# Optimization experiments

Measured on AMD Instinct MI355X. Metric: run time of the kernel, lower is better.

The kernel has to match this reference:

```python
import jax, jax.numpy as jnp
import numpy as np

N_DST = 25000
E = 400000
DN = 128   # dim_node
DE = 128   # dim_edge
DT = 128   # dim_time
DO = 128   # dim_out
H = 2      # num_head


def setup_inputs() -> dict:
    key = jax.random.key(0)
    ks = jax.random.split(key, 10)
    sc = 0.05
    node_h = jax.random.normal(ks[0], (N_DST + E, DN), jnp.float32)
    edge_f = jax.random.normal(ks[1], (E, DE), jnp.float32)
    dt = jax.random.uniform(ks[2], (E,), jnp.float32) * 100.0
    dst_idx = jax.random.randint(ks[3], (E,), 0, N_DST)
    # TimeEncode: Linear(1, dim_time) with w initialized to 1/10**linspace(0,9)
    time_w = jnp.asarray(1.0 / 10 ** np.linspace(0, 9, DT, dtype=np.float32))
    time_b = jnp.zeros((DT,), jnp.float32)
    Wq = jax.random.normal(ks[4], (DO, DN + DT), jnp.float32) * sc
    bq = jnp.zeros((DO,), jnp.float32)
    Wk = jax.random.normal(ks[5], (DO, DN + DE + DT), jnp.float32) * sc
    bk = jnp.zeros((DO,), jnp.float32)
    Wv = jax.random.normal(ks[6], (DO, DN + DE + DT), jnp.float32) * sc
    bv = jnp.zeros((DO,), jnp.float32)
    Wout = jax.random.normal(ks[7], (DO, DN + DO), jnp.float32) * sc
    bout = jnp.zeros((DO,), jnp.float32)
    gamma = jnp.ones((DO,), jnp.float32)
    beta = jnp.zeros((DO,), jnp.float32)
    return dict(node_h=node_h, edge_f=edge_f, dt=dt, dst_idx=dst_idx,
                time_w=time_w, time_b=time_b, Wq=Wq, bq=bq, Wk=Wk, bk=bk,
                Wv=Wv, bv=bv, Wout=Wout, bout=bout, gamma=gamma, beta=beta)


def reference(node_h, edge_f, dt, dst_idx, time_w, time_b,
              Wq, bq, Wk, bk, Wv, bv, Wout, bout, gamma, beta):
    num_dst = node_h.shape[0] - edge_f.shape[0]
    num_edges = edge_f.shape[0]
    tgt = node_h[:num_dst]            # [N, DN] target node embeddings
    src = node_h[num_dst:]            # [E, DN] per-edge source embeddings

    # TimeEncode: cos(w * dt + b)
    time_feats = jnp.cos(dt[:, None] * time_w[None, :] + time_b)          # [E, DT]
    zero_time = jnp.broadcast_to(jnp.cos(time_b), (num_dst, time_b.shape[0]))

    Qn = jnp.concatenate([tgt, zero_time], axis=1) @ Wq.T + bq            # [N, DO]
    kv_in = jnp.concatenate([src, edge_f, time_feats], axis=1)            # [E, DN+DE+DT]
    K = kv_in @ Wk.T + bk                                                 # [E, DO]
    V = kv_in @ Wv.T + bv                                                 # [E, DO]
    Q = Qn[dst_idx]                                                       # gather per edge

    d_head = Q.shape[1] // H
    Qh = Q.reshape(num_edges, H, d_head)
    Kh = K.reshape(num_edges, H, d_head)
    Vh = V.reshape(num_edges, H, d_head)

    score = jnp.sum(Qh * Kh, axis=2)                                      # [E, H]
    score = jnp.where(score >= 0, score, 0.2 * score)                     # LeakyReLU(0.2)

    # edge_softmax: segmented softmax over incoming edges of each dst node
    m = jax.ops.segment_max(score, dst_idx, num_segments=num_dst)
    m = jnp.where(jnp.isfinite(m), m, 0.0)                                # empty segments
    e = jnp.exp(score - m[dst_idx])
    s = jax.ops.segment_sum(e, dst_idx, num_segments=num_dst)
    att = e / s[dst_idx]                                                  # [E, H]

    Vw = (Vh * att[:, :, None]).reshape(num_edges, -1)                    # [E, DO]
    h = jax.ops.segment_sum(Vw, dst_idx, num_segments=num_dst)            # scatter-sum

    rst = jnp.concatenate([h, tgt], axis=1) @ Wout.T + bout               # [N, DO]
    rst = jax.nn.relu(rst)
    mu = jnp.mean(rst, axis=-1, keepdims=True)
    var = jnp.var(rst, axis=-1, keepdims=True)
    return (rst - mu) / jnp.sqrt(var + 1e-5) * gamma + beta
```

## Files before the change

kernel.cpp:

```cpp
#include <hip/hip_runtime.h>

#define N_DST 25000
#define E_NUM 400000

typedef __bf16 bf16x8 __attribute__((ext_vector_type(8)));
typedef __bf16 bf16x4 __attribute__((ext_vector_type(4)));
typedef float  f32x4  __attribute__((ext_vector_type(4)));

__device__ __forceinline__ float fast_cos(float x) {
  float r = x * 0.15915494309189535f;
  r = r - floorf(r);
  return __builtin_amdgcn_cosf(r);
}

__device__ __forceinline__ void pack_frag(const float* __restrict__ W0,
    const float* __restrict__ W1, int stride, int NC, int idx, __bf16* __restrict__ out) {
  int lane = idx & 63, fid = idx >> 6;
  int nfw = NC >> 6;
  int perks = nfw << 2;
  int ks = fid / perks, rem = fid - ks * perks;
  int w = rem / nfw, nf = rem - w * nfw;
  int n = w * (NC >> 2) + nf * 16 + (lane & 15);
  int g = (ks << 2) + (lane >> 4);
  const float* src = (W1 && n >= 128) ? (W1 + (size_t)(n - 128) * stride)
                                      : (W0 + (size_t)n * stride);
  const float4* s4 = reinterpret_cast<const float4*>(src + g * 8);
  float4 lo = s4[0], hi = s4[1];
  bf16x8 b;
  b[0]=(__bf16)lo.x; b[1]=(__bf16)lo.y; b[2]=(__bf16)lo.z; b[3]=(__bf16)lo.w;
  b[4]=(__bf16)hi.x; b[5]=(__bf16)hi.y; b[6]=(__bf16)hi.z; b[7]=(__bf16)hi.w;
  reinterpret_cast<bf16x8*>(out)[idx] = b;
}

__global__ __launch_bounds__(256) void prep_kernel(
    const float* __restrict__ Wq, const float* __restrict__ bq, const float* __restrict__ tb,
    const float* __restrict__ Wk, const float* __restrict__ Wv, const float* __restrict__ Wout,
    const int* __restrict__ dsti,
    float* __restrict__ cq, __bf16* __restrict__ Bq_kv, __bf16* __restrict__ Bq_q,
    __bf16* __restrict__ Bq_out, int* __restrict__ counts) {
  int b = blockIdx.x, tid = threadIdx.x;
  if (b == 0) {
    if (tid < 128) {
      float s = bq[tid];
      for (int j = 0; j < 128; ++j) s += cosf(tb[j]) * Wq[tid * 256 + 128 + j];
      cq[tid] = s;
    }
    return;
  }
  b -= 1;
  if (b < 48) { pack_frag(Wk, Wv, 384, 256, b * 256 + tid, Bq_kv); return; }
  b -= 48;
  if (b < 8)  { pack_frag(Wq, nullptr, 256, 128, b * 256 + tid, Bq_q); return; }
  b -= 8;
  if (b < 16) { pack_frag(Wout, nullptr, 256, 128, b * 256 + tid, Bq_out); return; }
  b -= 16;
  int e = b * 256 + tid;
  if (e < E_NUM) atomicAdd(&counts[dsti[e]], 1);
}

__global__ __launch_bounds__(1024) void scanA_kernel(const int* __restrict__ counts,
    int* __restrict__ bsum) {
  __shared__ int wsum[16];
  int tid = threadIdx.x;
  int idx = blockIdx.x * 1024 + tid;
  int s = (idx < N_DST) ? counts[idx] : 0;
#pragma unroll
  for (int o = 32; o; o >>= 1) s += __shfl_xor(s, o);
  if ((tid & 63) == 0) wsum[tid >> 6] = s;
  __syncthreads();
  if (tid == 0) {
    int t = 0;
#pragma unroll
    for (int i = 0; i < 16; ++i) t += wsum[i];
    bsum[blockIdx.x] = t;
  }
}

__global__ void scanB_kernel(const int* __restrict__ bsum, int* __restrict__ boff) {
  if (threadIdx.x == 0) {
    int c = 0;
    for (int i = 0; i < 25; ++i) { boff[i] = c; c += bsum[i]; }
    boff[25] = c;
  }
}

__global__ __launch_bounds__(1024) void scanC_kernel(const int* __restrict__ counts,
    const int* __restrict__ boff, int* __restrict__ offs, int* __restrict__ cursor) {
  __shared__ int wpart[16];
  int tid = threadIdx.x, lane = tid & 63, wid = tid >> 6;
  int idx = blockIdx.x * 1024 + tid;
  int x = (idx < N_DST) ? counts[idx] : 0;
  int incl = x;
#pragma unroll
  for (int o = 1; o < 64; o <<= 1) {
    int y = __shfl_up(incl, o);
    if (lane >= o) incl += y;
  }
  if (lane == 63) wpart[wid] = incl;
  __syncthreads();
  if (wid == 0) {
    int v = (lane < 16) ? wpart[lane] : 0;
    int s = v;
#pragma unroll
    for (int o = 1; o < 16; o <<= 1) {
      int y = __shfl_up(s, o);
      if (lane >= o) s += y;
    }
    if (lane < 16) wpart[lane] = s;
  }
  __syncthreads();
  int woff = (wid > 0) ? wpart[wid - 1] : 0;
  int v = boff[blockIdx.x] + woff + incl - x;
  if (idx < N_DST) {
    offs[idx] = v;
    cursor[idx] = v;
  }
  if (idx == N_DST - 1) offs[N_DST] = v + x;
}

__global__ __launch_bounds__(256) void fill_kernel(const int* __restrict__ dsti,
    int* __restrict__ cursor, int* __restrict__ elist, int* __restrict__ dsts) {
  int e = blockIdx.x * 256 + threadIdx.x;
  if (e < E_NUM) {
    int d = dsti[e];
    int p = atomicAdd(&cursor[d], 1);
    elist[p] = e;
    dsts[p] = d;
  }
}

#define WAITV(N) do { \
    asm volatile("s_waitcnt vmcnt(" #N ")" ::: "memory"); \
    __builtin_amdgcn_sched_barrier(0); } while (0)
#define PIPE_BAR() do { \
    asm volatile("s_waitcnt lgkmcnt(0)" ::: "memory"); \
    __builtin_amdgcn_sched_barrier(0); \
    __builtin_amdgcn_s_barrier(); \
    __builtin_amdgcn_sched_barrier(0); } while (0)

__global__ __launch_bounds__(256, 3) void kv_kernel(
    const float* __restrict__ node_h, const float* __restrict__ edge_f,
    const float* __restrict__ dtp, const float* __restrict__ tw, const float* __restrict__ tb,
    const __bf16* __restrict__ Bq,
    const float* __restrict__ bk, const float* __restrict__ bv,
    const int* __restrict__ elist, const int* __restrict__ dsts,
    const float* __restrict__ Qn,
    __bf16* __restrict__ Vout, float* __restrict__ score)
{
  __shared__ __align__(16) char SMEM[16384];
  __shared__ int Elds[64];
  __shared__ int Dlds[64];
  __shared__ float dts[64];
  __shared__ float twl[128];
  __shared__ float tbl[128];

  char* const Ab0 = SMEM;
  char* const Ab1 = SMEM + 8192;
  char* const Vlds = SMEM;

  const int tid = threadIdx.x;
  const int e0 = blockIdx.x * 64;
  const int lane = tid & 63;
  const int w = tid >> 6;
  const int lrow = lane & 15;
  const int lk = lane >> 4;
  const int aswz = (lrow & 7) << 4;

  if (tid < 64) {
    int e = elist[e0 + tid];
    Elds[tid] = e;
    Dlds[tid] = dsts[e0 + tid];
    dts[tid] = dtp[e];
  } else if (tid < 192) {
    int j = tid - 64;
    twl[j] = tw[j];
    tbl[j] = tb[j];
  }
  __syncthreads();

  const int srow = tid >> 2;
  const int sq = tid & 3;
  const int eidx = Elds[srow];
  const char* sR = (const char*)(node_h + (size_t)(N_DST + eidx) * 128) + sq * 64;
  const char* eR = (const char*)(edge_f + (size_t)eidx * 128) + sq * 64;

  float4 sA0, sA1, sA2, sA3, sB0, sB1, sB2, sB3;
#define ISSUE_STAGE(S0, S1, S2, S3, T) do { \
    const char* _p = ((T) < 2) ? (sR + (T) * 256) : (eR + ((T) - 2) * 256); \
    asm volatile("global_load_dwordx4 %0, %4, off\n\t" \
                 "global_load_dwordx4 %1, %4, off offset:16\n\t" \
                 "global_load_dwordx4 %2, %4, off offset:32\n\t" \
                 "global_load_dwordx4 %3, %4, off offset:48" \
                 : "=&v"(S0), "=&v"(S1), "=&v"(S2), "=&v"(S3) : "v"(_p)); } while (0)

  auto writeAt = [&](char* buf, float4 v0, float4 v1, float4 v2, float4 v3) {
    char* rb = buf + srow * 128;
    int sw = (srow & 7) << 4;
    float4 vv[4] = {v0, v1, v2, v3};
#pragma unroll
    for (int i = 0; i < 4; ++i) {
      bf16x4 b;
      b[0]=(__bf16)vv[i].x; b[1]=(__bf16)vv[i].y; b[2]=(__bf16)vv[i].z; b[3]=(__bf16)vv[i].w;
      *reinterpret_cast<bf16x4*>(rb + ((sq * 32 + i * 8) ^ sw)) = b;
    }
  };

  const bf16x8* __restrict__ Bw = reinterpret_cast<const bf16x8*>(Bq) + (size_t)(w * 4) * 64 + lane;
  float4 bq0, bq1, bq2, bq3, bq4, bq5, bq6, bq7;
#define ISSUE_B4(B0, B1, B2, B3, K32) do { \
    const void* _p = (const void*)(Bw + (size_t)(K32) * 16 * 64); \
    asm volatile("global_load_dwordx4 %0, %4, off\n\t" \
                 "global_load_dwordx4 %1, %4, off offset:1024\n\t" \
                 "global_load_dwordx4 %2, %4, off offset:2048\n\t" \
                 "global_load_dwordx4 %3, %4, off offset:3072" \
                 : "=&v"(B0), "=&v"(B1), "=&v"(B2), "=&v"(B3) : "v"(_p)); } while (0)
#define ISSUE_B8(T) do { ISSUE_B4(bq0, bq1, bq2, bq3, (T) * 2); \
                         ISSUE_B4(bq4, bq5, bq6, bq7, (T) * 2 + 1); } while (0)

  f32x4 acc[4][4];
#pragma unroll
  for (int mf = 0; mf < 4; ++mf)
#pragma unroll
    for (int nf = 0; nf < 4; ++nf)
      acc[mf][nf] = (f32x4){0.f, 0.f, 0.f, 0.f};

  float dv[4];
#pragma unroll
  for (int mf = 0; mf < 4; ++mf) dv[mf] = dts[mf * 16 + lrow];

  auto mfmaTile = [&](const char* buf) {
#pragma unroll
    for (int ks = 0; ks < 2; ++ks) {
#pragma unroll
      for (int mf = 0; mf < 4; ++mf) {
        bf16x8 a = *reinterpret_cast<const bf16x8*>(
            buf + (mf * 16 + lrow) * 128 + ((ks * 64 + lk * 16) ^ aswz));
        acc[mf][0] = __builtin_amdgcn_mfma_f32_16x16x32_bf16(a, __builtin_bit_cast(bf16x8, ks ? bq4 : bq0), acc[mf][0], 0, 0, 0);
        acc[mf][1] = __builtin_amdgcn_mfma_f32_16x16x32_bf16(a, __builtin_bit_cast(bf16x8, ks ? bq5 : bq1), acc[mf][1], 0, 0, 0);
        acc[mf][2] = __builtin_amdgcn_mfma_f32_16x16x32_bf16(a, __builtin_bit_cast(bf16x8, ks ? bq6 : bq2), acc[mf][2], 0, 0, 0);
        acc[mf][3] = __builtin_amdgcn_mfma_f32_16x16x32_bf16(a, __builtin_bit_cast(bf16x8, ks ? bq7 : bq3), acc[mf][3], 0, 0, 0);
      }
    }
  };

  ISSUE_STAGE(sA0, sA1, sA2, sA3, 0);
  ISSUE_STAGE(sB0, sB1, sB2, sB3, 1);
  WAITV(4);
  writeAt(Ab0, sA0, sA1, sA2, sA3);
  PIPE_BAR();
  ISSUE_B8(0);
  ISSUE_STAGE(sA0, sA1, sA2, sA3, 2);
  WAITV(4);
  mfmaTile(Ab0);
  writeAt(Ab1, sB0, sB1, sB2, sB3);
  PIPE_BAR();
  ISSUE_B8(1);
  ISSUE_STAGE(sB0, sB1, sB2, sB3, 3);
  WAITV(4);
  mfmaTile(Ab1);
  writeAt(Ab0, sA0, sA1, sA2, sA3);
  PIPE_BAR();
  ISSUE_B8(2);
  WAITV(0);
  mfmaTile(Ab0);
  writeAt(Ab1, sB0, sB1, sB2, sB3);
  PIPE_BAR();
  ISSUE_B8(3);
  WAITV(0);
  mfmaTile(Ab1);

  ISSUE_B4(bq0, bq1, bq2, bq3, 8);
#pragma unroll
  for (int cs = 0; cs < 4; ++cs) {
    if (cs == 0) ISSUE_B4(bq4, bq5, bq6, bq7, 9);
    else if (cs == 1) ISSUE_B4(bq0, bq1, bq2, bq3, 10);
    else if (cs == 2) ISSUE_B4(bq4, bq5, bq6, bq7, 11);
    int J = cs * 32 + lk * 8;
    f32x4 w0 = *reinterpret_cast<const f32x4*>(twl + J);
    f32x4 w1 = *reinterpret_cast<const f32x4*>(twl + J + 4);
    f32x4 c0 = *reinterpret_cast<const f32x4*>(tbl + J);
    f32x4 c1 = *reinterpret_cast<const f32x4*>(tbl + J + 4);
    bf16x8 a[4];
#pragma unroll
    for (int mf = 0; mf < 4; ++mf) {
      float d = dv[mf];
#pragma unroll
      for (int j = 0; j < 4; ++j) {
        a[mf][j] = (__bf16)fast_cos(d * w0[j] + c0[j]);
        a[mf][4 + j] = (__bf16)fast_cos(d * w1[j] + c1[j]);
      }
    }
    if (cs < 3) { WAITV(4); } else { WAITV(0); }
    bool lo = !(cs & 1);
    bf16x8 b0 = __builtin_bit_cast(bf16x8, lo ? bq0 : bq4);
    bf16x8 b1 = __builtin_bit_cast(bf16x8, lo ? bq1 : bq5);
    bf16x8 b2 = __builtin_bit_cast(bf16x8, lo ? bq2 : bq6);
    bf16x8 b3 = __builtin_bit_cast(bf16x8, lo ? bq3 : bq7);
#pragma unroll
    for (int mf = 0; mf < 4; ++mf) {
      acc[mf][0] = __builtin_amdgcn_mfma_f32_16x16x32_bf16(a[mf], b0, acc[mf][0], 0, 0, 0);
      acc[mf][1] = __builtin_amdgcn_mfma_f32_16x16x32_bf16(a[mf], b1, acc[mf][1], 0, 0, 0);
      acc[mf][2] = __builtin_amdgcn_mfma_f32_16x16x32_bf16(a[mf], b2, acc[mf][2], 0, 0, 0);
      acc[mf][3] = __builtin_amdgcn_mfma_f32_16x16x32_bf16(a[mf], b3, acc[mf][3], 0, 0, 0);
    }
  }

  PIPE_BAR();

  if (w >= 2) {
#pragma unroll
    for (int nf = 0; nf < 4; ++nf) {
      int vcol = (w - 2) * 64 + nf * 16 + lrow;
      float bb = bv[vcol];
#pragma unroll
      for (int mf = 0; mf < 4; ++mf) {
#pragma unroll
        for (int r = 0; r < 4; ++r) {
          int row = mf * 16 + lk * 4 + r;
          *reinterpret_cast<__bf16*>(Vlds + row * 256 + ((vcol * 2) ^ ((row & 7) << 4))) =
              (__bf16)(acc[mf][nf][r] + bb);
        }
      }
    }
  } else {
    float bkv[4];
#pragma unroll
    for (int nf = 0; nf < 4; ++nf) bkv[nf] = bk[w * 64 + nf * 16 + lrow];
#pragma unroll
    for (int mf = 0; mf < 4; ++mf) {
      float qv[4][4];
#pragma unroll
      for (int r = 0; r < 4; ++r) {
        const float* qrow = Qn + ((size_t)Dlds[mf * 16 + lk * 4 + r] << 7) + w * 64 + lrow;
#pragma unroll
        for (int nf = 0; nf < 4; ++nf)
          qv[r][nf] = qrow[nf * 16];
      }
#pragma unroll
      for (int r = 0; r < 4; ++r) {
        int row = mf * 16 + lk * 4 + r;
        float s = 0.f;
#pragma unroll
        for (int nf = 0; nf < 4; ++nf)
          s += (acc[mf][nf][r] + bkv[nf]) * qv[r][nf];
        s += __shfl_xor(s, 1);
        s += __shfl_xor(s, 2);
        s += __shfl_xor(s, 4);
        s += __shfl_xor(s, 8);
        if (lrow == 0) {
          s = (s >= 0.f) ? s : 0.2f * s;
          score[((size_t)(e0 + row) << 1) + w] = s;
        }
      }
    }
  }
  __syncthreads();
#pragma unroll
  for (int i = 0; i < 4; ++i) {
    int c = tid + i * 256;
    int r = c >> 4, cb = (c & 15) << 4;
    bf16x8 vv = *reinterpret_cast<const bf16x8*>(Vlds + r * 256 + (cb ^ ((r & 7) << 4)));
    *reinterpret_cast<bf16x8*>(Vout + (((size_t)(e0 + r)) << 7) + (c & 15) * 8) = vv;
  }
}

template<int MODE>
__global__ __launch_bounds__(256, 4) void gemm_kernel(
    const float* __restrict__ A0, const float* __restrict__ A1,
    const float* __restrict__ dtp, const float* __restrict__ tw,
    const __bf16* __restrict__ Bq, const float* __restrict__ bias0,
    float* __restrict__ outF)
{
  constexpr int NC = 128;
  constexpr int NFRAGW = 2;
  __shared__ __align__(16) char Abuf[2][64 * 256];

  const int tid = threadIdx.x;
  const int e0 = blockIdx.x * 64;
  const int nv = min(64, N_DST - e0);
  const int srow = tid >> 5;
  const int sc4 = (tid & 31) << 2;

  const int lane = tid & 63;
  const int w = tid >> 6;
  const int nbase = w * (NC / 4);
  const int lrow = lane & 15;
  const int lk = lane >> 4;
  const int aswz = (lrow & 7) << 4;
  const bf16x8* __restrict__ Bw =
      reinterpret_cast<const bf16x8*>(Bq) + (size_t)(w * NFRAGW) * 64 + lane;

  f32x4 acc[4][NFRAGW];
#pragma unroll
  for (int mf = 0; mf < 4; ++mf)
#pragma unroll
    for (int nf = 0; nf < NFRAGW; ++nf)
      acc[mf][nf] = (f32x4){0.f, 0.f, 0.f, 0.f};

  auto issueA = [&](int t, float4 (&v)[8]) {
    const float* base = (t == 0) ? A0 : A1;
#pragma unroll
    for (int i = 0; i < 8; ++i) {
      int r = srow + i * 8;
      v[i] = (r < nv) ? *reinterpret_cast<const float4*>(base + (size_t)(e0 + r) * 128 + sc4)
                      : make_float4(0.f, 0.f, 0.f, 0.f);
    }
  };
  auto writeA = [&](char* buf, float4 (&v)[8]) {
#pragma unroll
    for (int i = 0; i < 8; ++i) {
      int r = srow + i * 8;
      bf16x4 b;
      b[0]=(__bf16)v[i].x; b[1]=(__bf16)v[i].y; b[2]=(__bf16)v[i].z; b[3]=(__bf16)v[i].w;
      *reinterpret_cast<bf16x4*>(buf + r * 256 + ((sc4 * 2) ^ ((r & 7) << 4))) = b;
    }
  };
  auto ktile = [&](const char* buf, int t) {
#pragma unroll
    for (int ks = 0; ks < 4; ++ks) {
      bf16x8 b[NFRAGW];
#pragma unroll
      for (int nf = 0; nf < NFRAGW; ++nf)
        b[nf] = Bw[((size_t)(t * 4 + ks) * 4 * NFRAGW + nf) * 64];
      bf16x8 a[4];
#pragma unroll
      for (int mf = 0; mf < 4; ++mf)
        a[mf] = *reinterpret_cast<const bf16x8*>(
            buf + (mf * 16 + lrow) * 256 + (((ks * 32 + lk * 8) * 2) ^ aswz));
#pragma unroll
      for (int nf = 0; nf < NFRAGW; ++nf)
#pragma unroll
        for (int mf = 0; mf < 4; ++mf)
          acc[mf][nf] = __builtin_amdgcn_mfma_f32_16x16x32_bf16(a[mf], b[nf], acc[mf][nf], 0, 0, 0);
    }
  };

  float4 v[8];
  issueA(0, v);
  writeA(Abuf[0], v);
  __syncthreads();
  if constexpr (MODE == 2) {
    issueA(1, v);
    ktile(Abuf[0], 0);
    writeA(Abuf[1], v);
    __syncthreads();
    ktile(Abuf[1], 1);
  } else {
    ktile(Abuf[0], 0);
  }

  if constexpr (MODE == 0) {
#pragma unroll
    for (int nf = 0; nf < NFRAGW; ++nf) {
      int col = nbase + nf * 16 + lrow;
      float bb = bias0[col];
#pragma unroll
      for (int mf = 0; mf < 4; ++mf) {
#pragma unroll
        for (int r = 0; r < 4; ++r) {
          int row = mf * 16 + lk * 4 + r;
          if (row < nv)
            outF[(size_t)(e0 + row) * 128 + col] = acc[mf][nf][r] + bb;
        }
      }
    }
  } else {
    const float* gammaP = dtp;
    const float* betaP = tw;
    float vals[NFRAGW][4][4];
#pragma unroll
    for (int nf = 0; nf < NFRAGW; ++nf) {
      float bb = bias0[nbase + nf * 16 + lrow];
#pragma unroll
      for (int mf = 0; mf < 4; ++mf)
#pragma unroll
        for (int r = 0; r < 4; ++r)
          vals[nf][mf][r] = fmaxf(acc[mf][nf][r] + bb, 0.f);
    }
    __syncthreads();
    float* sums = reinterpret_cast<float*>(Abuf[0]);
    float* sqs  = reinterpret_cast<float*>(Abuf[0]) + 256;
    float* stats = reinterpret_cast<float*>(Abuf[0]) + 512;
#pragma unroll
    for (int mf = 0; mf < 4; ++mf) {
#pragma unroll
      for (int r = 0; r < 4; ++r) {
        float s1 = vals[0][mf][r] + vals[1][mf][r];
        float s2 = vals[0][mf][r] * vals[0][mf][r] + vals[1][mf][r] * vals[1][mf][r];
#pragma unroll
        for (int o = 1; o < 16; o <<= 1) {
          s1 += __shfl_xor(s1, o);
          s2 += __shfl_xor(s2, o);
        }
        if (lrow == 0) {
          int row = mf * 16 + lk * 4 + r;
          sums[w * 64 + row] = s1;
          sqs[w * 64 + row] = s2;
        }
      }
    }
    __syncthreads();
    if (tid < 64) {
      float s = sums[tid] + sums[64 + tid] + sums[128 + tid] + sums[192 + tid];
      float q = sqs[tid] + sqs[64 + tid] + sqs[128 + tid] + sqs[192 + tid];
      float mean = s * (1.f / 128.f);
      float var = q * (1.f / 128.f) - mean * mean;
      stats[tid * 2] = mean;
      stats[tid * 2 + 1] = rsqrtf(var + 1e-5f);
    }
    __syncthreads();
#pragma unroll
    for (int nf = 0; nf < NFRAGW; ++nf) {
      int col = nbase + nf * 16 + lrow;
      float g = gammaP[col], bC = betaP[col];
#pragma unroll
      for (int mf = 0; mf < 4; ++mf) {
#pragma unroll
        for (int r = 0; r < 4; ++r) {
          int row = mf * 16 + lk * 4 + r;
          if (row < nv) {
            float mean = stats[row * 2], rs = stats[row * 2 + 1];
            outF[(size_t)(e0 + row) * 128 + col] = (vals[nf][mf][r] - mean) * rs * g + bC;
          }
        }
      }
    }
  }
}

__global__ __launch_bounds__(256) void agg_kernel(const int* __restrict__ offs,
    const float* __restrict__ score, const __bf16* __restrict__ V, float* __restrict__ h) {
  int d = blockIdx.x * 4 + (threadIdx.x >> 6);
  if (d >= N_DST) return;
  int lane = threadIdx.x & 63;
  int beg = offs[d], end = offs[d + 1];
  int n = end - beg;
  float m0 = -3.0e38f, m1 = -3.0e38f;
  for (int i = lane; i < n; i += 64) {
    float2 sc = *reinterpret_cast<const float2*>(score + 2 * (size_t)(beg + i));
    m0 = fmaxf(m0, sc.x); m1 = fmaxf(m1, sc.y);
  }
#pragma unroll
  for (int o = 32; o; o >>= 1) {
    m0 = fmaxf(m0, __shfl_xor(m0, o));
    m1 = fmaxf(m1, __shfl_xor(m1, o));
  }
  float s0 = 0.f, s1 = 0.f;
  for (int i = lane; i < n; i += 64) {
    float2 sc = *reinterpret_cast<const float2*>(score + 2 * (size_t)(beg + i));
    s0 += __expf(sc.x - m0); s1 += __expf(sc.y - m1);
  }
#pragma unroll
  for (int o = 32; o; o >>= 1) {
    s0 += __shfl_xor(s0, o);
    s1 += __shfl_xor(s1, o);
  }
  float inv0 = (n > 0) ? 1.f / s0 : 0.f;
  float inv1 = (n > 0) ? 1.f / s1 : 0.f;
  int q = lane >> 4, j = lane & 15;
  int hsel = j >> 3;
  float acc[8];
#pragma unroll
  for (int k2 = 0; k2 < 8; ++k2) acc[k2] = 0.f;
  for (int i0 = 0; i0 < n; i0 += 4) {
    int i = i0 + q;
    if (i < n) {
      size_t p = beg + i;
      float2 sc = *reinterpret_cast<const float2*>(score + 2 * p);
      float wgt = hsel ? __expf(sc.y - m1) * inv1 : __expf(sc.x - m0) * inv0;
      bf16x8 v = *reinterpret_cast<const bf16x8*>(V + (p << 7) + j * 8);
#pragma unroll
      for (int k2 = 0; k2 < 8; ++k2) acc[k2] += wgt * (float)v[k2];
    }
  }
#pragma unroll
  for (int k2 = 0; k2 < 8; ++k2) {
    acc[k2] += __shfl_xor(acc[k2], 16);
    acc[k2] += __shfl_xor(acc[k2], 32);
  }
  if (q == 0) {
    float4 lo = make_float4(acc[0], acc[1], acc[2], acc[3]);
    float4 hi = make_float4(acc[4], acc[5], acc[6], acc[7]);
    float* dst = h + ((size_t)d << 7) + j * 8;
    *reinterpret_cast<float4*>(dst) = lo;
    *reinterpret_cast<float4*>(dst + 4) = hi;
  }
}

extern "C" void kernel_launch(void* const* d_in, const int* in_sizes, int n_in,
                              void* d_out, int out_size, void* d_ws, size_t ws_size,
                              hipStream_t stream) {
  (void)in_sizes; (void)n_in; (void)out_size; (void)ws_size;
  const float* node_h = (const float*)d_in[0];
  const float* edge_f = (const float*)d_in[1];
  const float* dtp    = (const float*)d_in[2];
  const int*   dsti   = (const int*)d_in[3];
  const float* tw     = (const float*)d_in[4];
  const float* tb     = (const float*)d_in[5];
  const float* Wq     = (const float*)d_in[6];
  const float* bq     = (const float*)d_in[7];
  const float* Wk     = (const float*)d_in[8];
  const float* bk     = (const float*)d_in[9];
  const float* Wv     = (const float*)d_in[10];
  const float* bv     = (const float*)d_in[11];
  const float* Wout   = (const float*)d_in[12];
  const float* bout   = (const float*)d_in[13];
  const float* gamma  = (const float*)d_in[14];
  const float* beta   = (const float*)d_in[15];
  float* outp = (float*)d_out;

  size_t off = 0;
  auto take = [&](size_t nbytes) -> void* {
    void* r = (char*)d_ws + off;
    off += (nbytes + 255) & ~(size_t)255;
    return r;
  };
  __bf16* Bq_kv  = (__bf16*)take((size_t)12288 * 16);
  __bf16* Bq_q   = (__bf16*)take((size_t)2048 * 16);
  __bf16* Bq_out = (__bf16*)take((size_t)4096 * 16);
  float*  cq     = (float*)take(128 * 4);
  float*  Qn     = (float*)take((size_t)N_DST * 128 * 4);
  __bf16* Vbuf   = (__bf16*)take((size_t)E_NUM * 128 * 2);
  float*  score  = (float*)take((size_t)E_NUM * 2 * 4);
  int*    counts = (int*)take((size_t)N_DST * 4);
  int*    offs   = (int*)take((size_t)(N_DST + 1) * 4);
  int*    cursor = (int*)take((size_t)N_DST * 4);
  int*    elist  = (int*)take((size_t)E_NUM * 4);
  int*    dsts   = (int*)take((size_t)E_NUM * 4);
  int*    bsum   = (int*)take(32 * 4);
  int*    boff   = (int*)take(32 * 4);
  float*  hbuf   = (float*)take((size_t)N_DST * 128 * 4);

  hipMemsetAsync(counts, 0, (size_t)N_DST * 4, stream);

  const int count_blocks = (E_NUM + 255) / 256;
  prep_kernel<<<1 + 48 + 8 + 16 + count_blocks, 256, 0, stream>>>(
      Wq, bq, tb, Wk, Wv, Wout, dsti, cq, Bq_kv, Bq_q, Bq_out, counts);

  gemm_kernel<0><<<(N_DST + 63) / 64, 256, 0, stream>>>(node_h, nullptr, nullptr, nullptr,
      Bq_q, cq, Qn);

  scanA_kernel<<<25, 1024, 0, stream>>>(counts, bsum);
  scanB_kernel<<<1, 64, 0, stream>>>(bsum, boff);
  scanC_kernel<<<25, 1024, 0, stream>>>(counts, boff, offs, cursor);
  fill_kernel<<<count_blocks, 256, 0, stream>>>(dsti, cursor, elist, dsts);

  kv_kernel<<<E_NUM / 64, 256, 0, stream>>>(node_h, edge_f, dtp, tw, tb,
      Bq_kv, bk, bv, elist, dsts, Qn, Vbuf, score);

  agg_kernel<<<(N_DST + 3) / 4, 256, 0, stream>>>(offs, score, Vbuf, hbuf);

  gemm_kernel<2><<<(N_DST + 63) / 64, 256, 0, stream>>>(hbuf, node_h, gamma, beta,
      Bq_out, bout, outp);
}
```

Measured before the change: 332.1 us.

## Double-buffer weight fragment loads in kv_kernel and lower occupancy target

The kernel now keeps two register sets for the B (weight) fragments, so the next tile's weights are prefetched one stage ahead and the full vmcnt(0) waits on the critical path go away. It also relaxes launch bounds from 3 to 2 waves per SIMD so the extra 32 VGPRs fit without spilling. The trade is lower occupancy, which may reduce latency hiding for the gather loads, in exchange for deeper software pipelining.

```diff
diff --git a/kernel.cpp b/kernel.cpp
--- a/kernel.cpp
+++ b/kernel.cpp
@@ -138,7 +138,7 @@
     __builtin_amdgcn_s_barrier(); \
     __builtin_amdgcn_sched_barrier(0); } while (0)
 
-__global__ __launch_bounds__(256, 3) void kv_kernel(
+__global__ __launch_bounds__(256, 2) void kv_kernel(
     const float* __restrict__ node_h, const float* __restrict__ edge_f,
     const float* __restrict__ dtp, const float* __restrict__ tw, const float* __restrict__ tb,
     const __bf16* __restrict__ Bq,
@@ -206,7 +206,8 @@
   };
 
   const bf16x8* __restrict__ Bw = reinterpret_cast<const bf16x8*>(Bq) + (size_t)(w * 4) * 64 + lane;
-  float4 bq0, bq1, bq2, bq3, bq4, bq5, bq6, bq7;
+  float4 qa0, qa1, qa2, qa3, qa4, qa5, qa6, qa7;
+  float4 qb0, qb1, qb2, qb3, qb4, qb5, qb6, qb7;
 #define ISSUE_B4(B0, B1, B2, B3, K32) do { \
     const void* _p = (const void*)(Bw + (size_t)(K32) * 16 * 64); \
     asm volatile("global_load_dwordx4 %0, %4, off\n\t" \
@@ -214,8 +215,10 @@
                  "global_load_dwordx4 %2, %4, off offset:2048\n\t" \
                  "global_load_dwordx4 %3, %4, off offset:3072" \
                  : "=&v"(B0), "=&v"(B1), "=&v"(B2), "=&v"(B3) : "v"(_p)); } while (0)
-#define ISSUE_B8(T) do { ISSUE_B4(bq0, bq1, bq2, bq3, (T) * 2); \
-                         ISSUE_B4(bq4, bq5, bq6, bq7, (T) * 2 + 1); } while (0)
+#define ISSUE_B8A(T) do { ISSUE_B4(qa0, qa1, qa2, qa3, (T) * 2); \
+                          ISSUE_B4(qa4, qa5, qa6, qa7, (T) * 2 + 1); } while (0)
+#define ISSUE_B8B(T) do { ISSUE_B4(qb0, qb1, qb2, qb3, (T) * 2); \
+                          ISSUE_B4(qb4, qb5, qb6, qb7, (T) * 2 + 1); } while (0)
 
   f32x4 acc[4][4];
 #pragma unroll
@@ -228,53 +231,67 @@
 #pragma unroll
   for (int mf = 0; mf < 4; ++mf) dv[mf] = dts[mf * 16 + lrow];
 
-  auto mfmaTile = [&](const char* buf) {
+  auto mfmaTileA = [&](const char* buf) {
 #pragma unroll
     for (int ks = 0; ks < 2; ++ks) {
 #pragma unroll
       for (int mf = 0; mf < 4; ++mf) {
         bf16x8 a = *reinterpret_cast<const bf16x8*>(
             buf + (mf * 16 + lrow) * 128 + ((ks * 64 + lk * 16) ^ aswz));
-        acc[mf][0] = __builtin_amdgcn_mfma_f32_16x16x32_bf16(a, __builtin_bit_cast(bf16x8, ks ? bq4 : bq0), acc[mf][0], 0, 0, 0);
-        acc[mf][1] = __builtin_amdgcn_mfma_f32_16x16x32_bf16(a, __builtin_bit_cast(bf16x8, ks ? bq5 : bq1), acc[mf][1], 0, 0, 0);
-        acc[mf][2] = __builtin_amdgcn_mfma_f32_16x16x32_bf16(a, __builtin_bit_cast(bf16x8, ks ? bq6 : bq2), acc[mf][2], 0, 0, 0);
-        acc[mf][3] = __builtin_amdgcn_mfma_f32_16x16x32_bf16(a, __builtin_bit_cast(bf16x8, ks ? bq7 : bq3), acc[mf][3], 0, 0, 0);
+        acc[mf][0] = __builtin_amdgcn_mfma_f32_16x16x32_bf16(a, __builtin_bit_cast(bf16x8, ks ? qa4 : qa0), acc[mf][0], 0, 0, 0);
+        acc[mf][1] = __builtin_amdgcn_mfma_f32_16x16x32_bf16(a, __builtin_bit_cast(bf16x8, ks ? qa5 : qa1), acc[mf][1], 0, 0, 0);
+        acc[mf][2] = __builtin_amdgcn_mfma_f32_16x16x32_bf16(a, __builtin_bit_cast(bf16x8, ks ? qa6 : qa2), acc[mf][2], 0, 0, 0);
+        acc[mf][3] = __builtin_amdgcn_mfma_f32_16x16x32_bf16(a, __builtin_bit_cast(bf16x8, ks ? qa7 : qa3), acc[mf][3], 0, 0, 0);
+      }
+    }
+  };
+  auto mfmaTileB = [&](const char* buf) {
+#pragma unroll
+    for (int ks = 0; ks < 2; ++ks) {
+#pragma unroll
+      for (int mf = 0; mf < 4; ++mf) {
+        bf16x8 a = *reinterpret_cast<const bf16x8*>(
+            buf + (mf * 16 + lrow) * 128 + ((ks * 64 + lk * 16) ^ aswz));
+        acc[mf][0] = __builtin_amdgcn_mfma_f32_16x16x32_bf16(a, __builtin_bit_cast(bf16x8, ks ? qb4 : qb0), acc[mf][0], 0, 0, 0);
+        acc[mf][1] = __builtin_amdgcn_mfma_f32_16x16x32_bf16(a, __builtin_bit_cast(bf16x8, ks ? qb5 : qb1), acc[mf][1], 0, 0, 0);
+        acc[mf][2] = __builtin_amdgcn_mfma_f32_16x16x32_bf16(a, __builtin_bit_cast(bf16x8, ks ? qb6 : qb2), acc[mf][2], 0, 0, 0);
+        acc[mf][3] = __builtin_amdgcn_mfma_f32_16x16x32_bf16(a, __builtin_bit_cast(bf16x8, ks ? qb7 : qb3), acc[mf][3], 0, 0, 0);
       }
     }
   };
 
   ISSUE_STAGE(sA0, sA1, sA2, sA3, 0);
   ISSUE_STAGE(sB0, sB1, sB2, sB3, 1);
-  WAITV(4);
+  ISSUE_B8A(0);
+  WAITV(12);
   writeAt(Ab0, sA0, sA1, sA2, sA3);
   PIPE_BAR();
-  ISSUE_B8(0);
+  ISSUE_B8B(1);
   ISSUE_STAGE(sA0, sA1, sA2, sA3, 2);
-  WAITV(4);
-  mfmaTile(Ab0);
+  WAITV(12);
+  mfmaTileA(Ab0);
   writeAt(Ab1, sB0, sB1, sB2, sB3);
   PIPE_BAR();
-  ISSUE_B8(1);
+  ISSUE_B8A(2);
   ISSUE_STAGE(sB0, sB1, sB2, sB3, 3);
-  WAITV(4);
-  mfmaTile(Ab1);
+  WAITV(12);
+  mfmaTileB(Ab1);
   writeAt(Ab0, sA0, sA1, sA2, sA3);
   PIPE_BAR();
-  ISSUE_B8(2);
-  WAITV(0);
-  mfmaTile(Ab0);
+  ISSUE_B8B(3);
+  WAITV(8);
+  mfmaTileA(Ab0);
   writeAt(Ab1, sB0, sB1, sB2, sB3);
   PIPE_BAR();
-  ISSUE_B8(3);
-  WAITV(0);
-  mfmaTile(Ab1);
-
-  ISSUE_B4(bq0, bq1, bq2, bq3, 8);
+  ISSUE_B4(qa0, qa1, qa2, qa3, 8);
+  ISSUE_B4(qa4, qa5, qa6, qa7, 9);
+  WAITV(8);
+  mfmaTileB(Ab1);
+
 #pragma unroll
   for (int cs = 0; cs < 4; ++cs) {
-    if (cs == 0) ISSUE_B4(bq4, bq5, bq6, bq7, 9);
-    else if (cs == 1) ISSUE_B4(bq0, bq1, bq2, bq3, 10);
-    else if (cs == 2) ISSUE_B4(bq4, bq5, bq6, bq7, 11);
+    if (cs == 0) ISSUE_B4(qb0, qb1, qb2, qb3, 10);
+    else if (cs == 1) ISSUE_B4(qb4, qb5, qb6, qb7, 11);
     int J = cs * 32 + lk * 8;
     f32x4 w0 = *reinterpret_cast<const f32x4*>(twl + J);
     f32x4 w1 = *reinterpret_cast<const f32x4*>(twl + J + 4);
@@ -290,12 +307,15 @@
         a[mf][4 + j] = (__bf16)fast_cos(d * w1[j] + c1[j]);
       }
     }
-    if (cs < 3) { WAITV(4); } else { WAITV(0); }
-    bool lo = !(cs & 1);
-    bf16x8 b0 = __builtin_bit_cast(bf16x8, lo ? bq0 : bq4);
-    bf16x8 b1 = __builtin_bit_cast(bf16x8, lo ? bq1 : bq5);
-    bf16x8 b2 = __builtin_bit_cast(bf16x8, lo ? bq2 : bq6);
-    bf16x8 b3 = __builtin_bit_cast(bf16x8, lo ? bq3 : bq7);
+    if (cs == 0) { WAITV(8); }
+    else if (cs == 1) { WAITV(8); }
+    else if (cs == 2) { WAITV(4); }
+    else { WAITV(0); }
+    bf16x8 b0, b1, b2, b3;
+    if (cs == 0) { b0 = __builtin_bit_cast(bf16x8, qa0); b1 = __builtin_bit_cast(bf16x8, qa1); b2 = __builtin_bit_cast(bf16x8, qa2); b3 = __builtin_bit_cast(bf16x8, qa3); }
+    else if (cs == 1) { b0 = __builtin_bit_cast(bf16x8, qa4); b1 = __builtin_bit_cast(bf16x8, qa5); b2 = __builtin_bit_cast(bf16x8, qa6); b3 = __builtin_bit_cast(bf16x8, qa7); }
+    else if (cs == 2) { b0 = __builtin_bit_cast(bf16x8, qb0); b1 = __builtin_bit_cast(bf16x8, qb1); b2 = __builtin_bit_cast(bf16x8, qb2); b3 = __builtin_bit_cast(bf16x8, qb3); }
+    else { b0 = __builtin_bit_cast(bf16x8, qb4); b1 = __builtin_bit_cast(bf16x8, qb5); b2 = __builtin_bit_cast(bf16x8, qb6); b3 = __builtin_bit_cast(bf16x8, qb7); }
 #pragma unroll
     for (int mf = 0; mf < 4; ++mf) {
       acc[mf][0] = __builtin_amdgcn_mfma_f32_16x16x32_bf16(a[mf], b0, acc[mf][0], 0, 0, 0);
```

Result: slower. 341.4 us, median of 2 (+2.8%).
